# Optimization experiments

Hardware: AMD Instinct MI355X
Metric: run time of the kernel (lower is better)

The kernel has to match this reference:

```python
import jax, jax.numpy as jnp
import numpy as np

ALPHA = 0.01  # LeakyReLU negative slope
NEG_INF = -1e12  # same masking constant as the torch code


def setup_inputs() -> dict:
    key = jax.random.key(0)
    k1, k2, k3, k4 = jax.random.split(key, 4)
    B, N, C_IN, C_OUT = 8, 2048, 128, 64
    inp = jax.random.normal(k1, (B, N, C_IN), dtype=jnp.float32)
    adj = jax.random.randint(k2, (N, N), 0, 2).astype(jnp.float32)
    # xavier_uniform with gain=1.414
    def xavier(k, shape, gain=1.414):
        fan_in, fan_out = shape[0], shape[1]
        limit = gain * np.sqrt(6.0 / (fan_in + fan_out))
        return jax.random.uniform(k, shape, jnp.float32, -limit, limit)
    W = xavier(k3, (C_IN, C_OUT))
    a = xavier(k4, (2 * C_OUT, 1))
    return {"inp": inp, "adj": adj, "W": W, "a": a}


def reference(inp, adj, W, a):
    # inp: [B, N, C_in], adj: [N, N], W: [C_in, F], a: [2F, 1]
    B, N, _ = inp.shape
    F_out = W.shape[1]
    adj = adj + jnp.eye(N, dtype=adj.dtype)  # add self-loops
    h = jnp.einsum('bnc,cf->bnf', inp, W)    # [B, N, F]
    # a^T [h_i || h_j] = <a1, h_i> + <a2, h_j>  (identical math, no NxNx2F tensor)
    a1 = a[:F_out, 0]
    a2 = a[F_out:, 0]
    s1 = h @ a1  # [B, N] score contribution of source node i
    s2 = h @ a2  # [B, N] score contribution of target node j
    e = jax.nn.leaky_relu(s1[:, :, None] + s2[:, None, :], negative_slope=ALPHA)  # [B, N, N]
    att = jnp.where(adj[None, :, :] > 0, e, NEG_INF)
    att = jax.nn.softmax(att, axis=2)
    h_prime = jnp.einsum('bnm,bmf->bnf', att, h)  # [B, N, F]
    return h_prime
```

## Files before the change

### kernel.cpp

```cpp
#include <hip/hip_runtime.h>
#include <hip/hip_bf16.h>
#include <cstddef>
#include <cstdint>


#define B_DIM 8
#define N_DIM 2048
#define C_IN  128
#define C_OUT 64
#define NROWS (B_DIM * N_DIM)
#define LOG2E 1.4426950408889634f

typedef short bf16x8 __attribute__((ext_vector_type(8)));
typedef short bf16x4 __attribute__((ext_vector_type(4)));
typedef float f32x4  __attribute__((ext_vector_type(4)));

static __device__ __forceinline__ short f2bf(float x) {
    __hip_bfloat16 b = __float2bfloat16(x);
    return *reinterpret_cast<short*>(&b);
}

__global__ __launch_bounds__(256) void gat_prep(
    const float* __restrict__ inp,
    const float* __restrict__ W,
    const float* __restrict__ a,
    const float* __restrict__ adj,
    __hip_bfloat16* __restrict__ hT,
    float* __restrict__ E1, float* __restrict__ F1,
    float* __restrict__ E2, float* __restrict__ F2,
    unsigned long long* __restrict__ mask)
{
    __shared__ float Wl[C_IN * C_OUT];
    __shared__ float a1l[C_OUT], a2l[C_OUT];
    __shared__ float tr[C_OUT][17];

    if (blockIdx.x >= 1024) {
        const int i    = blockIdx.x - 1024;
        const int wave = threadIdx.x >> 6;
        const int lane = threadIdx.x & 63;
        const float* __restrict__ arow = adj + (size_t)i * N_DIM;
#pragma unroll
        for (int it = 0; it < 8; ++it) {
            const int j = wave * 512 + it * 64 + lane;
            const bool conn = (arow[j] > 0.f) || (j == i);
            const unsigned long long bm = __ballot(conn);
            if (lane == 0) mask[(size_t)i * (N_DIM / 64) + (j >> 6)] = bm;
        }
        return;
    }

    {
        const float4* Wv = (const float4*)W;
        float4* Wd = (float4*)Wl;
        for (int t = threadIdx.x; t < C_IN * C_OUT / 4; t += 256) Wd[t] = Wv[t];
        if (threadIdx.x < C_OUT) {
            a1l[threadIdx.x] = a[threadIdx.x];
            a2l[threadIdx.x] = a[C_OUT + threadIdx.x];
        }
    }
    __syncthreads();

    const int wave = threadIdx.x >> 6;
    const int lane = threadIdx.x & 63;
    const int i0 = blockIdx.x * 16;
    const int b  = i0 >> 11;
    const int il = i0 & (N_DIM - 1);
    const int rl = wave * 4;

    const float* __restrict__ x0 = inp + (size_t)(i0 + rl) * C_IN;
    const float* __restrict__ x1 = x0 + C_IN;
    const float* __restrict__ x2 = x1 + C_IN;
    const float* __restrict__ x3 = x2 + C_IN;
    float h0 = 0.f, h1 = 0.f, h2 = 0.f, h3 = 0.f;
#pragma unroll 4
    for (int c = 0; c < C_IN; c += 4) {
        const float4 a0 = *(const float4*)(x0 + c);
        const float4 a1 = *(const float4*)(x1 + c);
        const float4 a2 = *(const float4*)(x2 + c);
        const float4 a3 = *(const float4*)(x3 + c);
#pragma unroll
        for (int cc = 0; cc < 4; ++cc) {
            const float w_ = Wl[(c + cc) * C_OUT + lane];
            const float e0 = (cc==0)?a0.x:(cc==1)?a0.y:(cc==2)?a0.z:a0.w;
            const float e1 = (cc==0)?a1.x:(cc==1)?a1.y:(cc==2)?a1.z:a1.w;
            const float e2 = (cc==0)?a2.x:(cc==1)?a2.y:(cc==2)?a2.z:a2.w;
            const float e3 = (cc==0)?a3.x:(cc==1)?a3.y:(cc==2)?a3.z:a3.w;
            h0 = fmaf(e0, w_, h0);
            h1 = fmaf(e1, w_, h1);
            h2 = fmaf(e2, w_, h2);
            h3 = fmaf(e3, w_, h3);
        }
    }
    tr[lane][rl + 0] = h0;
    tr[lane][rl + 1] = h1;
    tr[lane][rl + 2] = h2;
    tr[lane][rl + 3] = h3;

    float hv[4] = {h0, h1, h2, h3};
#pragma unroll
    for (int k = 0; k < 4; ++k) {
        float p1 = hv[k] * a1l[lane];
        float p2 = hv[k] * a2l[lane];
#pragma unroll
        for (int off = 32; off; off >>= 1) {
            p1 += __shfl_xor(p1, off, 64);
            p2 += __shfl_xor(p2, off, 64);
        }
        if (lane == 0) {
            const float z1 = p1 * LOG2E;
            const float z2 = p2 * LOG2E;
            const int r = i0 + rl + k;
            E1[r] = exp2f(z1);
            F1[r] = exp2f(0.01f * z1);
            E2[r] = exp2f(z2);
            F2[r] = exp2f(0.01f * z2);
        }
    }
    __syncthreads();

    const int f   = threadIdx.x >> 2;
    const int ro4 = (threadIdx.x & 3) * 4;
    bf16x4 v;
    v[0] = f2bf(tr[f][ro4 + 0]);
    v[1] = f2bf(tr[f][ro4 + 1]);
    v[2] = f2bf(tr[f][ro4 + 2]);
    v[3] = f2bf(tr[f][ro4 + 3]);
    *(bf16x4*)(hT + ((size_t)b * C_OUT + f) * N_DIM + il + ro4) = v;
}

__global__ __launch_bounds__(512, 4) void gat_attn(
    const __hip_bfloat16* __restrict__ hT,
    const float* __restrict__ E1, const float* __restrict__ F1,
    const float* __restrict__ E2, const float* __restrict__ F2,
    const unsigned long long* __restrict__ mask,
    float* __restrict__ out)
{
    __shared__ __align__(16) char smem[2][32768];
    __shared__ float lred[8][16];

    const int wave = threadIdx.x >> 6;
    const int lane = threadIdx.x & 63;
    const int half = wave >> 2;
    const int jq   = wave & 3;
    const int tb = blockIdx.x;
    const int b  = tb >> 6;
    const int i0 = (tb & 63) * 32;
    const int mloc = lane & 15;
    const int quad = lane >> 4;
    const int i_g  = i0 + half * 16 + mloc;

    const float E1v = E1[(size_t)b * N_DIM + i_g];
    const float F1v = F1[(size_t)b * N_DIM + i_g];
    const float* __restrict__ E2b = E2 + (size_t)b * N_DIM;
    const float* __restrict__ F2b = F2 + (size_t)b * N_DIM;
    const uint8_t* __restrict__ mB = (const uint8_t*)mask;
    const char* __restrict__ hTb = (const char*)(hT + (size_t)b * C_OUT * N_DIM);

    f32x4 acc0 = {0.f,0.f,0.f,0.f}, acc1 = {0.f,0.f,0.f,0.f};
    f32x4 acc2 = {0.f,0.f,0.f,0.f}, acc3 = {0.f,0.f,0.f,0.f};
    f32x4 accl = {0.f,0.f,0.f,0.f};
    const bf16x8 ones = {(short)0x3F80, (short)0x3F80, (short)0x3F80, (short)0x3F80,
                         (short)0x3F80, (short)0x3F80, (short)0x3F80, (short)0x3F80};

    auto compute_chunk = [&](int jc, const char* buf) {
#pragma unroll
        for (int st = 0; st < 2; ++st) {
            const int bjl = jq * 64 + st * 32 + quad * 8;
            const int jg  = jc * 256 + bjl;
            const int cA  = bjl >> 3;
            const unsigned mb = mB[(size_t)i_g * (N_DIM / 8) + (jg >> 3)];
            const f32x4 eA = *(const f32x4*)(E2b + jg);
            const f32x4 eB = *(const f32x4*)(E2b + jg + 4);
            const f32x4 fA = *(const f32x4*)(F2b + jg);
            const f32x4 fB = *(const f32x4*)(F2b + jg + 4);
            bf16x8 pf;
#pragma unroll
            for (int t = 0; t < 8; ++t) {
                const float pe = E1v * (t < 4 ? eA[t] : eB[t - 4]);
                const float pn = F1v * (t < 4 ? fA[t] : fB[t - 4]);
                float p = fmaxf(pe, pn);
                p = ((mb >> t) & 1u) ? p : 0.f;
                pf[t] = f2bf(p);
            }
            accl = __builtin_amdgcn_mfma_f32_16x16x32_bf16(pf, ones, accl, 0, 0, 0);
#pragma unroll
            for (int nb = 0; nb < 4; ++nb) {
                const int f  = nb * 16 + mloc;
                const int cS = (cA & 16) | ((cA ^ (f & 15)) & 15);
                const bf16x8 bF = *(const bf16x8*)(buf + (f * 32 + cS) * 16);
                if (nb == 0) acc0 = __builtin_amdgcn_mfma_f32_16x16x32_bf16(pf, bF, acc0, 0, 0, 0);
                if (nb == 1) acc1 = __builtin_amdgcn_mfma_f32_16x16x32_bf16(pf, bF, acc1, 0, 0, 0);
                if (nb == 2) acc2 = __builtin_amdgcn_mfma_f32_16x16x32_bf16(pf, bF, acc2, 0, 0, 0);
                if (nb == 3) acc3 = __builtin_amdgcn_mfma_f32_16x16x32_bf16(pf, bF, acc3, 0, 0, 0);
            }
        }
    };

    for (int jc = 0; jc < 8; ++jc) {
        __syncthreads();
#pragma unroll
        for (int q = 0; q < 4; ++q) {
            const int p = (wave * 4 + q) * 64 + lane;
            const int f  = p >> 5;
            const int cs = p & 31;
            const int c  = (cs & 16) | ((cs ^ (f & 15)) & 15);
            const char* gp = hTb + ((size_t)f * N_DIM + jc * 256) * 2 + c * 16;
            char* lp = smem[jc & 1] + (wave * 4 + q) * 1024;
            __builtin_amdgcn_global_load_lds(
                (const __attribute__((address_space(1))) void*)gp,
                (__attribute__((address_space(3))) void*)lp, 16, 0, 0);
        }
        if (jc > 0) compute_chunk(jc - 1, smem[(jc - 1) & 1]);
    }
    __syncthreads();
    compute_chunk(7, smem[1]);
    __syncthreads();

    if (mloc == 0) {
#pragma unroll
        for (int reg = 0; reg < 4; ++reg)
            lred[wave][quad * 4 + reg] = accl[reg];
    }

    float* accL = (float*)smem[0];
#pragma unroll
    for (int reg = 0; reg < 4; ++reg) {
        const int r = quad * 4 + reg;
        accL[(wave * 16 + r) * 64 + 0 * 16 + mloc] = acc0[reg];
        accL[(wave * 16 + r) * 64 + 1 * 16 + mloc] = acc1[reg];
        accL[(wave * 16 + r) * 64 + 2 * 16 + mloc] = acc2[reg];
        accL[(wave * 16 + r) * 64 + 3 * 16 + mloc] = acc3[reg];
    }
    __syncthreads();

    float* __restrict__ ob = out + ((size_t)b * N_DIM + i0) * C_OUT;
#pragma unroll
    for (int e = threadIdx.x; e < 32 * C_OUT; e += 512) {
        const int R = e >> 6;
        const int hf = R >> 4;
        const int r  = R & 15;
        float s = 0.f, ls = 0.f;
#pragma unroll
        for (int q = 0; q < 4; ++q) {
            const int w = hf * 4 + q;
            s  += accL[(w * 16 + r) * 64 + (e & 63)];
            ls += lred[w][r];
        }
        ob[e] = s / ls;
    }
}

extern "C" void kernel_launch(void* const* d_in, const int* in_sizes, int n_in,
                              void* d_out, int out_size, void* d_ws, size_t ws_size,
                              hipStream_t stream) {
    const float* inp = (const float*)d_in[0];
    const float* adj = (const float*)d_in[1];
    const float* W   = (const float*)d_in[2];
    const float* a   = (const float*)d_in[3];
    float* out = (float*)d_out;

    char* ws = (char*)d_ws;
    __hip_bfloat16* hT = (__hip_bfloat16*)ws;
    float* E1 = (float*)(ws + (size_t)2 * 1024 * 1024);
    float* F1 = E1 + NROWS;
    float* E2 = F1 + NROWS;
    float* F2 = E2 + NROWS;
    unsigned long long* mask = (unsigned long long*)(F2 + NROWS);

    gat_prep<<<1024 + N_DIM, 256, 0, stream>>>(inp, W, a, adj, hT, E1, F1, E2, F2, mask);
    gat_attn<<<NROWS / 32, 512, 0, stream>>>(hT, E1, F1, E2, F2, mask, out);
}
```

Baseline: 117.0 us.

## Process more rows per prep block with a transposed W layout and fewer blocks

The prep kernel now computes 32 rows per block (8 per wave) instead of 16, so each W load from shared memory is reused across more rows. W is stored in LDS in a transposed layout so each lane reads a float4 of four input channels at once. The mask-building blocks each handle 4 adjacency rows, which cuts the grid from 3072 to 1024 blocks and amortises W staging over more work. The trade-off is more registers per thread and fewer blocks available to hide latency.

After: 122.9 us. 5.0% more time.

```diff
diff --git a/kernel.cpp b/kernel.cpp
--- a/kernel.cpp
+++ b/kernel.cpp
@@ -30,77 +30,66 @@
     float* __restrict__ E2, float* __restrict__ F2,
     unsigned long long* __restrict__ mask)
 {
-    __shared__ float Wl[C_IN * C_OUT];
+    __shared__ float Wt2[32 * 256];
     __shared__ float a1l[C_OUT], a2l[C_OUT];
-    __shared__ float tr[C_OUT][17];
-
-    if (blockIdx.x >= 1024) {
-        const int i    = blockIdx.x - 1024;
-        const int wave = threadIdx.x >> 6;
-        const int lane = threadIdx.x & 63;
-        const float* __restrict__ arow = adj + (size_t)i * N_DIM;
-#pragma unroll
-        for (int it = 0; it < 8; ++it) {
-            const int j = wave * 512 + it * 64 + lane;
-            const bool conn = (arow[j] > 0.f) || (j == i);
-            const unsigned long long bm = __ballot(conn);
-            if (lane == 0) mask[(size_t)i * (N_DIM / 64) + (j >> 6)] = bm;
-        }
-        return;
-    }
-
-    {
-        const float4* Wv = (const float4*)W;
-        float4* Wd = (float4*)Wl;
-        for (int t = threadIdx.x; t < C_IN * C_OUT / 4; t += 256) Wd[t] = Wv[t];
-        if (threadIdx.x < C_OUT) {
-            a1l[threadIdx.x] = a[threadIdx.x];
-            a2l[threadIdx.x] = a[C_OUT + threadIdx.x];
-        }
-    }
-    __syncthreads();
+    __shared__ float tr[C_OUT][33];
 
     const int wave = threadIdx.x >> 6;
     const int lane = threadIdx.x & 63;
-    const int i0 = blockIdx.x * 16;
+
+    if (blockIdx.x >= 512) {
+        const int ib = (blockIdx.x - 512) * 4;
+#pragma unroll
+        for (int r = 0; r < 4; ++r) {
+            const int i = ib + r;
+            const float* __restrict__ arow = adj + (size_t)i * N_DIM;
+#pragma unroll
+            for (int it = 0; it < 8; ++it) {
+                const int j = wave * 512 + it * 64 + lane;
+                const bool conn = (arow[j] > 0.f) || (j == i);
+                const unsigned long long bm = __ballot(conn);
+                if (lane == 0) mask[(size_t)i * (N_DIM / 64) + (j >> 6)] = bm;
+            }
+        }
+        return;
+    }
+
+    for (int t = threadIdx.x; t < C_IN * C_OUT; t += 256) {
+        const int c = t >> 6, f = t & 63;
+        Wt2[((c >> 2) << 8) + (f << 2) + (c & 3)] = W[t];
+    }
+    if (threadIdx.x < C_OUT) {
+        a1l[threadIdx.x] = a[threadIdx.x];
+        a2l[threadIdx.x] = a[C_OUT + threadIdx.x];
+    }
+    __syncthreads();
+
+    const int i0 = blockIdx.x * 32;
     const int b  = i0 >> 11;
     const int il = i0 & (N_DIM - 1);
-    const int rl = wave * 4;
-
-    const float* __restrict__ x0 = inp + (size_t)(i0 + rl) * C_IN;
-    const float* __restrict__ x1 = x0 + C_IN;
-    const float* __restrict__ x2 = x1 + C_IN;
-    const float* __restrict__ x3 = x2 + C_IN;
-    float h0 = 0.f, h1 = 0.f, h2 = 0.f, h3 = 0.f;
-#pragma unroll 4
-    for (int c = 0; c < C_IN; c += 4) {
-        const float4 a0 = *(const float4*)(x0 + c);
-        const float4 a1 = *(const float4*)(x1 + c);
-        const float4 a2 = *(const float4*)(x2 + c);
-        const float4 a3 = *(const float4*)(x3 + c);
-#pragma unroll
-        for (int cc = 0; cc < 4; ++cc) {
-            const float w_ = Wl[(c + cc) * C_OUT + lane];
-            const float e0 = (cc==0)?a0.x:(cc==1)?a0.y:(cc==2)?a0.z:a0.w;
-            const float e1 = (cc==0)?a1.x:(cc==1)?a1.y:(cc==2)?a1.z:a1.w;
-            const float e2 = (cc==0)?a2.x:(cc==1)?a2.y:(cc==2)?a2.z:a2.w;
-            const float e3 = (cc==0)?a3.x:(cc==1)?a3.y:(cc==2)?a3.z:a3.w;
-            h0 = fmaf(e0, w_, h0);
-            h1 = fmaf(e1, w_, h1);
-            h2 = fmaf(e2, w_, h2);
-            h3 = fmaf(e3, w_, h3);
-        }
-    }
-    tr[lane][rl + 0] = h0;
-    tr[lane][rl + 1] = h1;
-    tr[lane][rl + 2] = h2;
-    tr[lane][rl + 3] = h3;
-
-    float hv[4] = {h0, h1, h2, h3};
-#pragma unroll
-    for (int k = 0; k < 4; ++k) {
-        float p1 = hv[k] * a1l[lane];
-        float p2 = hv[k] * a2l[lane];
+    const int rl = wave * 8;
+
+    const float* __restrict__ xp = inp + (size_t)(i0 + rl) * C_IN;
+    float hacc[8] = {0.f,0.f,0.f,0.f,0.f,0.f,0.f,0.f};
+#pragma unroll 2
+    for (int g = 0; g < 32; ++g) {
+        const float4 wv = *(const float4*)&Wt2[(g << 8) + (lane << 2)];
+#pragma unroll
+        for (int r = 0; r < 8; ++r) {
+            const float4 xv = *(const float4*)(xp + r * C_IN + g * 4);
+            hacc[r] = fmaf(xv.x, wv.x, hacc[r]);
+            hacc[r] = fmaf(xv.y, wv.y, hacc[r]);
+            hacc[r] = fmaf(xv.z, wv.z, hacc[r]);
+            hacc[r] = fmaf(xv.w, wv.w, hacc[r]);
+        }
+    }
+#pragma unroll
+    for (int r = 0; r < 8; ++r) tr[lane][rl + r] = hacc[r];
+
+#pragma unroll
+    for (int r = 0; r < 8; ++r) {
+        float p1 = hacc[r] * a1l[lane];
+        float p2 = hacc[r] * a2l[lane];
 #pragma unroll
         for (int off = 32; off; off >>= 1) {
             p1 += __shfl_xor(p1, off, 64);
@@ -109,23 +98,27 @@
         if (lane == 0) {
             const float z1 = p1 * LOG2E;
             const float z2 = p2 * LOG2E;
-            const int r = i0 + rl + k;
-            E1[r] = exp2f(z1);
-            F1[r] = exp2f(0.01f * z1);
-            E2[r] = exp2f(z2);
-            F2[r] = exp2f(0.01f * z2);
-        }
-    }
-    __syncthreads();
-
-    const int f   = threadIdx.x >> 2;
-    const int ro4 = (threadIdx.x & 3) * 4;
-    bf16x4 v;
-    v[0] = f2bf(tr[f][ro4 + 0]);
-    v[1] = f2bf(tr[f][ro4 + 1]);
-    v[2] = f2bf(tr[f][ro4 + 2]);
-    v[3] = f2bf(tr[f][ro4 + 3]);
-    *(bf16x4*)(hT + ((size_t)b * C_OUT + f) * N_DIM + il + ro4) = v;
+            const int rr = i0 + rl + r;
+            E1[rr] = exp2f(z1);
+            F1[rr] = exp2f(0.01f * z1);
+            E2[rr] = exp2f(z2);
+            F2[rr] = exp2f(0.01f * z2);
+        }
+    }
+    __syncthreads();
+
+#pragma unroll
+    for (int it = 0; it < 2; ++it) {
+        const int idx = it * 256 + threadIdx.x;
+        const int f   = idx >> 3;
+        const int ro4 = (idx & 7) * 4;
+        bf16x4 v;
+        v[0] = f2bf(tr[f][ro4 + 0]);
+        v[1] = f2bf(tr[f][ro4 + 1]);
+        v[2] = f2bf(tr[f][ro4 + 2]);
+        v[3] = f2bf(tr[f][ro4 + 3]);
+        *(bf16x4*)(hT + ((size_t)b * C_OUT + f) * N_DIM + il + ro4) = v;
+    }
 }
 
 __global__ __launch_bounds__(512, 4) void gat_attn(
@@ -267,6 +260,6 @@
     float* F2 = E2 + NROWS;
     unsigned long long* mask = (unsigned long long*)(F2 + NROWS);
 
-    gat_prep<<<1024 + N_DIM, 256, 0, stream>>>(inp, W, a, adj, hT, E1, F1, E2, F2, mask);
+    gat_prep<<<1024, 256, 0, stream>>>(inp, W, a, adj, hT, E1, F1, E2, F2, mask);
     gat_attn<<<NROWS / 32, 512, 0, stream>>>(hT, E1, F1, E2, F2, mask, out);
 }
```

## Remap waves so each covers both row halves over a narrower column slice

Applied to the files above, without the earlier changes.

Each of the 8 waves now computes both 16-row halves of the 32-row block over a 32-column slice of each chunk, instead of one half over 64 columns. Each LDS B-fragment read and each E2/F2 vector load now feeds two MFMAs, one per row half, which cuts LDS and global traffic per MFMA. The cost is twice as many accumulator registers per wave. The final cross-wave reduction also grows from 4 to 8 partials per row, and its staging buffer now fills the whole shared-memory array.

Result: faster. 112.7 us, median of 2 (-3.7%).

```diff
diff --git a/kernel.cpp b/kernel.cpp
--- a/kernel.cpp
+++ b/kernel.cpp
@@ -136,63 +136,72 @@
     float* __restrict__ out)
 {
     __shared__ __align__(16) char smem[2][32768];
-    __shared__ float lred[8][16];
+    __shared__ float lred[8][2][16];
 
     const int wave = threadIdx.x >> 6;
     const int lane = threadIdx.x & 63;
-    const int half = wave >> 2;
-    const int jq   = wave & 3;
     const int tb = blockIdx.x;
     const int b  = tb >> 6;
     const int i0 = (tb & 63) * 32;
     const int mloc = lane & 15;
     const int quad = lane >> 4;
-    const int i_g  = i0 + half * 16 + mloc;
-
-    const float E1v = E1[(size_t)b * N_DIM + i_g];
-    const float F1v = F1[(size_t)b * N_DIM + i_g];
+    const int igA  = i0 + mloc;
+    const int igB  = i0 + 16 + mloc;
+
+    const float E1A = E1[(size_t)b * N_DIM + igA];
+    const float F1A = F1[(size_t)b * N_DIM + igA];
+    const float E1B = E1[(size_t)b * N_DIM + igB];
+    const float F1B = F1[(size_t)b * N_DIM + igB];
     const float* __restrict__ E2b = E2 + (size_t)b * N_DIM;
     const float* __restrict__ F2b = F2 + (size_t)b * N_DIM;
-    const uint8_t* __restrict__ mB = (const uint8_t*)mask;
+    const uint8_t* __restrict__ mA = (const uint8_t*)mask + (size_t)igA * (N_DIM / 8);
+    const uint8_t* __restrict__ mBp = (const uint8_t*)mask + (size_t)igB * (N_DIM / 8);
     const char* __restrict__ hTb = (const char*)(hT + (size_t)b * C_OUT * N_DIM);
 
-    f32x4 acc0 = {0.f,0.f,0.f,0.f}, acc1 = {0.f,0.f,0.f,0.f};
-    f32x4 acc2 = {0.f,0.f,0.f,0.f}, acc3 = {0.f,0.f,0.f,0.f};
-    f32x4 accl = {0.f,0.f,0.f,0.f};
+    f32x4 aA0 = {0,0,0,0}, aA1 = {0,0,0,0}, aA2 = {0,0,0,0}, aA3 = {0,0,0,0};
+    f32x4 aB0 = {0,0,0,0}, aB1 = {0,0,0,0}, aB2 = {0,0,0,0}, aB3 = {0,0,0,0};
+    f32x4 lA = {0,0,0,0}, lB = {0,0,0,0};
     const bf16x8 ones = {(short)0x3F80, (short)0x3F80, (short)0x3F80, (short)0x3F80,
                          (short)0x3F80, (short)0x3F80, (short)0x3F80, (short)0x3F80};
 
+    const int bjl = wave * 32 + quad * 8;
+    const int cA  = bjl >> 3;
+
     auto compute_chunk = [&](int jc, const char* buf) {
-#pragma unroll
-        for (int st = 0; st < 2; ++st) {
-            const int bjl = jq * 64 + st * 32 + quad * 8;
-            const int jg  = jc * 256 + bjl;
-            const int cA  = bjl >> 3;
-            const unsigned mb = mB[(size_t)i_g * (N_DIM / 8) + (jg >> 3)];
-            const f32x4 eA = *(const f32x4*)(E2b + jg);
-            const f32x4 eB = *(const f32x4*)(E2b + jg + 4);
-            const f32x4 fA = *(const f32x4*)(F2b + jg);
-            const f32x4 fB = *(const f32x4*)(F2b + jg + 4);
-            bf16x8 pf;
-#pragma unroll
-            for (int t = 0; t < 8; ++t) {
-                const float pe = E1v * (t < 4 ? eA[t] : eB[t - 4]);
-                const float pn = F1v * (t < 4 ? fA[t] : fB[t - 4]);
-                float p = fmaxf(pe, pn);
-                p = ((mb >> t) & 1u) ? p : 0.f;
-                pf[t] = f2bf(p);
-            }
-            accl = __builtin_amdgcn_mfma_f32_16x16x32_bf16(pf, ones, accl, 0, 0, 0);
-#pragma unroll
-            for (int nb = 0; nb < 4; ++nb) {
-                const int f  = nb * 16 + mloc;
-                const int cS = (cA & 16) | ((cA ^ (f & 15)) & 15);
-                const bf16x8 bF = *(const bf16x8*)(buf + (f * 32 + cS) * 16);
-                if (nb == 0) acc0 = __builtin_amdgcn_mfma_f32_16x16x32_bf16(pf, bF, acc0, 0, 0, 0);
-                if (nb == 1) acc1 = __builtin_amdgcn_mfma_f32_16x16x32_bf16(pf, bF, acc1, 0, 0, 0);
-                if (nb == 2) acc2 = __builtin_amdgcn_mfma_f32_16x16x32_bf16(pf, bF, acc2, 0, 0, 0);
-                if (nb == 3) acc3 = __builtin_amdgcn_mfma_f32_16x16x32_bf16(pf, bF, acc3, 0, 0, 0);
-            }
+        const int jg = jc * 256 + bjl;
+        const unsigned mbA = mA[jg >> 3];
+        const unsigned mbB = mBp[jg >> 3];
+        const f32x4 eA = *(const f32x4*)(E2b + jg);
+        const f32x4 eB = *(const f32x4*)(E2b + jg + 4);
+        const f32x4 fA = *(const f32x4*)(F2b + jg);
+        const f32x4 fB = *(const f32x4*)(F2b + jg + 4);
+        bf16x8 pf0, pf1;
+#pragma unroll
+        for (int t = 0; t < 8; ++t) {
+            const float ev = (t < 4 ? eA[t] : eB[t - 4]);
+            const float fv = (t < 4 ? fA[t] : fB[t - 4]);
+            float p0 = fmaxf(E1A * ev, F1A * fv);
+            p0 = ((mbA >> t) & 1u) ? p0 : 0.f;
+            pf0[t] = f2bf(p0);
+            float p1 = fmaxf(E1B * ev, F1B * fv);
+            p1 = ((mbB >> t) & 1u) ? p1 : 0.f;
+            pf1[t] = f2bf(p1);
+        }
+        lA = __builtin_amdgcn_mfma_f32_16x16x32_bf16(pf0, ones, lA, 0, 0, 0);
+        lB = __builtin_amdgcn_mfma_f32_16x16x32_bf16(pf1, ones, lB, 0, 0, 0);
+#pragma unroll
+        for (int nb = 0; nb < 4; ++nb) {
+            const int f  = nb * 16 + mloc;
+            const int cS = (cA & 16) | ((cA ^ (f & 15)) & 15);
+            const bf16x8 bF = *(const bf16x8*)(buf + (f * 32 + cS) * 16);
+            if (nb == 0) { aA0 = __builtin_amdgcn_mfma_f32_16x16x32_bf16(pf0, bF, aA0, 0, 0, 0);
+                           aB0 = __builtin_amdgcn_mfma_f32_16x16x32_bf16(pf1, bF, aB0, 0, 0, 0); }
+            if (nb == 1) { aA1 = __builtin_amdgcn_mfma_f32_16x16x32_bf16(pf0, bF, aA1, 0, 0, 0);
+                           aB1 = __builtin_amdgcn_mfma_f32_16x16x32_bf16(pf1, bF, aB1, 0, 0, 0); }
+            if (nb == 2) { aA2 = __builtin_amdgcn_mfma_f32_16x16x32_bf16(pf0, bF, aA2, 0, 0, 0);
+                           aB2 = __builtin_amdgcn_mfma_f32_16x16x32_bf16(pf1, bF, aB2, 0, 0, 0); }
+            if (nb == 3) { aA3 = __builtin_amdgcn_mfma_f32_16x16x32_bf16(pf0, bF, aA3, 0, 0, 0);
+                           aB3 = __builtin_amdgcn_mfma_f32_16x16x32_bf16(pf1, bF, aB3, 0, 0, 0); }
         }
     };
 
@@ -218,33 +227,35 @@
 
     if (mloc == 0) {
 #pragma unroll
-        for (int reg = 0; reg < 4; ++reg)
-            lred[wave][quad * 4 + reg] = accl[reg];
-    }
-
-    float* accL = (float*)smem[0];
+        for (int reg = 0; reg < 4; ++reg) {
+            lred[wave][0][quad * 4 + reg] = lA[reg];
+            lred[wave][1][quad * 4 + reg] = lB[reg];
+        }
+    }
+
+    float* accL = (float*)smem;
 #pragma unroll
     for (int reg = 0; reg < 4; ++reg) {
         const int r = quad * 4 + reg;
-        accL[(wave * 16 + r) * 64 + 0 * 16 + mloc] = acc0[reg];
-        accL[(wave * 16 + r) * 64 + 1 * 16 + mloc] = acc1[reg];
-        accL[(wave * 16 + r) * 64 + 2 * 16 + mloc] = acc2[reg];
-        accL[(wave * 16 + r) * 64 + 3 * 16 + mloc] = acc3[reg];
+        float* pa = accL + ((wave * 2 + 0) * 16 + r) * 64 + mloc;
+        float* pb = accL + ((wave * 2 + 1) * 16 + r) * 64 + mloc;
+        pa[ 0] = aA0[reg]; pa[16] = aA1[reg]; pa[32] = aA2[reg]; pa[48] = aA3[reg];
+        pb[ 0] = aB0[reg]; pb[16] = aB1[reg]; pb[32] = aB2[reg]; pb[48] = aB3[reg];
     }
     __syncthreads();
 
     float* __restrict__ ob = out + ((size_t)b * N_DIM + i0) * C_OUT;
 #pragma unroll
     for (int e = threadIdx.x; e < 32 * C_OUT; e += 512) {
-        const int R = e >> 6;
+        const int R  = e >> 6;
         const int hf = R >> 4;
         const int r  = R & 15;
+        const int fc = e & 63;
         float s = 0.f, ls = 0.f;
 #pragma unroll
-        for (int q = 0; q < 4; ++q) {
-            const int w = hf * 4 + q;
-            s  += accL[(w * 16 + r) * 64 + (e & 63)];
-            ls += lred[w][r];
+        for (int w = 0; w < 8; ++w) {
+            s  += accL[((w * 2 + hf) * 16 + r) * 64 + fc];
+            ls += lred[w][hf][r];
         }
         ob[e] = s / ls;
     }
```
